# Performance work log

Hardware: AMD Instinct MI355X
Metric: run time of the kernel (lower is better)

## Reference

```python
import jax, jax.numpy as jnp
import numpy as np

# --- model dims (match init_kwargs) ---
B, N = 2, 4096          # batch, seq_len
D = 1024                # model dim
H, DH = 16, 64          # heads, dim_head (inner = H*DH = D)
R = 64                  # num_random_features
L = 6                   # depth
FF = 4 * D              # ff_dim
V = 32000               # vocab_size
MAXN = 4096             # max_seq_len
EPS = 1e-5              # torch LayerNorm default eps
STAB = 1e-6             # numerical_stabilizer
INNER = H * DH


def _ln(x, g, b):
    m = jnp.mean(x, axis=-1, keepdims=True)
    v = jnp.mean(jnp.square(x - m), axis=-1, keepdims=True)
    return (x - m) * jax.lax.rsqrt(v + EPS) * g + b


def setup_inputs() -> dict:
    key = jax.random.key(0)
    ks = jax.random.split(key, 16)
    s = 0.02
    return {
        "tokens": jax.random.randint(ks[0], (B, N), 0, V),
        "tok_emb": jax.random.normal(ks[1], (V, D), jnp.float32) * s,
        "pos_emb": jax.random.normal(ks[2], (MAXN, D), jnp.float32) * s,
        "Wqkv": jax.random.normal(ks[3], (L, 3 * INNER, D), jnp.float32) * s,
        "Wout": jax.random.normal(ks[4], (L, D, INNER), jnp.float32) * s,
        "bout": jnp.zeros((L, D), jnp.float32),
        "ln1_g": jnp.ones((L, D), jnp.float32),
        "ln1_b": jnp.zeros((L, D), jnp.float32),
        "ln2_g": jnp.ones((L, D), jnp.float32),
        "ln2_b": jnp.zeros((L, D), jnp.float32),
        "W1": jax.random.normal(ks[5], (L, FF, D), jnp.float32) * s,
        "b1": jnp.zeros((L, FF), jnp.float32),
        "W2": jax.random.normal(ks[6], (L, D, FF), jnp.float32) * s,
        "b2": jnp.zeros((L, D), jnp.float32),
        # random_features buffer: randn / sqrt(R)
        "rf": jax.random.normal(ks[7], (L, H, DH, R), jnp.float32) / np.sqrt(R),
    }


def reference(tokens, tok_emb, pos_emb, Wqkv, Wout, bout,
              ln1_g, ln1_b, ln2_g, ln2_b, W1, b1, W2, b2, rf):
    b, n = tokens.shape
    x = tok_emb[tokens] + pos_emb[jnp.arange(n)][None]  # [b,n,D]
    for l in range(L):
        # --- Performer attention (FAVOR+ linear path, ReLU kernel) ---
        h = _ln(x, ln1_g[l], ln1_b[l])
        qkv = h @ Wqkv[l].T                                  # [b,n,3*INNER]
        q, k, v = jnp.split(qkv, 3, axis=-1)
        resh = lambda t: t.reshape(b, n, H, DH).transpose(0, 2, 1, 3)  # [b,h,n,d]
        q, k, v = resh(q), resh(k), resh(v)
        phi_q = jax.nn.relu(jnp.einsum('bhnd,hdr->bhnr', q, rf[l]))
        phi_k = jax.nn.relu(jnp.einsum('bhnd,hdr->bhnr', k, rf[l]))
        kv = jnp.einsum('bhnr,bhnd->bhrd', phi_k, v)          # [b,h,r,d]
        out = jnp.einsum('bhnr,bhrd->bhnd', phi_q, kv)        # [b,h,n,d]
        # normalizer = phi_q . (sum_m phi_k)
        normz = jnp.einsum('bhnr,bhr->bhn', phi_q, phi_k.sum(axis=2))[..., None] + STAB
        out = out / normz
        out = out.transpose(0, 2, 1, 3).reshape(b, n, INNER)
        x = x + (out @ Wout[l].T + bout[l])
        # --- FFN (GELU exact, matching torch nn.GELU) ---
        h2 = _ln(x, ln2_g[l], ln2_b[l])
        ff = jax.nn.gelu(h2 @ W1[l].T + b1[l], approximate=False) @ W2[l].T + b2[l]
        x = x + ff
    return x
```

## Files before the change

kernel.cpp:

```cpp
#include <hip/hip_runtime.h>
#include <hip/hip_bf16.h>
#include <math.h>

#define NL 6
#define DMODEL 1024
#define NHEAD 16
#define MTOT 8192
#define NSEQ 4096
#define FFDIM 4096

typedef __attribute__((ext_vector_type(8))) short bf16x8;
typedef __attribute__((ext_vector_type(4))) short s16x4;
typedef __attribute__((ext_vector_type(4))) float f32x4;

__device__ __forceinline__ float b2f(short s) {
    unsigned int u = ((unsigned int)(unsigned short)s) << 16;
    return __uint_as_float(u);
}
__device__ __forceinline__ short f2b(float f) {
    __hip_bfloat16 h = __float2bfloat16(f);
    return *reinterpret_cast<short*>(&h);
}
__device__ __forceinline__ f32x4 mfma16(bf16x8 a, bf16x8 b, f32x4 c) {
    return __builtin_amdgcn_mfma_f32_16x16x32_bf16(a, b, c, 0, 0, 0);
}
__device__ __forceinline__ void gload16(const void* g, void* lds) {
    __builtin_amdgcn_global_load_lds((__attribute__((address_space(1))) void*)(g),
                                     (__attribute__((address_space(3))) void*)(lds), 16, 0, 0);
}

__global__ __launch_bounds__(256) void cvt_f2b_kernel(const float* __restrict__ in,
        short* __restrict__ out, int n4) {
    int i = blockIdx.x * 256 + threadIdx.x;
    if (i >= n4) return;
    float4 v = ((const float4*)in)[i];
    s16x4 o;
    o[0] = f2b(v.x); o[1] = f2b(v.y); o[2] = f2b(v.z); o[3] = f2b(v.w);
    ((s16x4*)out)[i] = o;
}

__global__ __launch_bounds__(256) void embed_kernel(const int* __restrict__ tok,
        const float* __restrict__ te, const float* __restrict__ pe, float* __restrict__ x) {
    int row = blockIdx.x, tid = threadIdx.x;
    int t = tok[row], n = row & (NSEQ - 1);
    float4 a = ((const float4*)(te + (size_t)t * DMODEL))[tid];
    float4 p = ((const float4*)(pe + (size_t)n * DMODEL))[tid];
    float4 o;
    o.x = a.x + p.x; o.y = a.y + p.y; o.z = a.z + p.z; o.w = a.w + p.w;
    ((float4*)(x + (size_t)row * DMODEL))[tid] = o;
}

__global__ __launch_bounds__(256) void prep_phi(const float* __restrict__ Wqkv,
        const float* __restrict__ rf, short* __restrict__ Wcomb) {
    int b = blockIdx.x;
    int kc = b & 3, qk = (b >> 2) & 1, h = (b >> 3) & 15, l = b >> 7;
    int tid = threadIdx.x;
    __shared__ float rfl[64 * 64];
    const float* rfg = rf + ((size_t)(l * NHEAD + h)) * 4096;
    #pragma unroll
    for (int u = 0; u < 4; u++) {
        int i4 = u * 256 + tid;
        ((float4*)rfl)[i4] = ((const float4*)rfg)[i4];
    }
    __syncthreads();
    int k = kc * 256 + tid;
    const float* wq = Wqkv + ((size_t)(l * 3072 + qk * 1024 + h * 64)) * DMODEL + k;
    float acc[64];
    #pragma unroll
    for (int r = 0; r < 64; r++) acc[r] = 0.f;
    #pragma unroll 4
    for (int d = 0; d < 64; d++) {
        float wd = wq[(size_t)d * DMODEL];
        const float4* rrow = (const float4*)&rfl[d * 64];
        #pragma unroll
        for (int r4 = 0; r4 < 16; r4++) {
            float4 f = rrow[r4];
            acc[r4 * 4 + 0] += f.x * wd;
            acc[r4 * 4 + 1] += f.y * wd;
            acc[r4 * 4 + 2] += f.z * wd;
            acc[r4 * 4 + 3] += f.w * wd;
        }
    }
    size_t outbase = ((size_t)(l * 3072 + qk * 1024 + h * 64)) * DMODEL + k;
    #pragma unroll
    for (int r = 0; r < 64; r++)
        Wcomb[outbase + (size_t)r * DMODEL] = f2b(acc[r]);
}

__global__ __launch_bounds__(256) void prep_v(const float* __restrict__ Wqkv,
        short* __restrict__ Wcomb) {
    int b = blockIdx.x;
    int l = b >> 10, row = b & 1023;
    int tid = threadIdx.x;
    size_t base = ((size_t)(l * 3072 + 2048 + row)) * DMODEL;
    float4 v = ((const float4*)(Wqkv + base))[tid];
    s16x4 o;
    o[0] = f2b(v.x); o[1] = f2b(v.y); o[2] = f2b(v.z); o[3] = f2b(v.w);
    ((s16x4*)(Wcomb + base))[tid] = o;
}

__global__ __launch_bounds__(256) void ln_kernel(const float* __restrict__ x,
        const float* __restrict__ g, const float* __restrict__ bta, short* __restrict__ h) {
    int row = blockIdx.x, tid = threadIdx.x, lane = tid & 63, w = tid >> 6;
    float4 v = ((const float4*)(x + (size_t)row * DMODEL))[tid];
    float s = v.x + v.y + v.z + v.w;
    float sq = v.x * v.x + v.y * v.y + v.z * v.z + v.w * v.w;
    #pragma unroll
    for (int off = 32; off > 0; off >>= 1) { s += __shfl_down(s, off); sq += __shfl_down(sq, off); }
    __shared__ float ss[4], sqq[4];
    if (lane == 0) { ss[w] = s; sqq[w] = sq; }
    __syncthreads();
    float st = ss[0] + ss[1] + ss[2] + ss[3];
    float sqt = sqq[0] + sqq[1] + sqq[2] + sqq[3];
    float mean = st * (1.f / 1024.f);
    float var = sqt * (1.f / 1024.f) - mean * mean;
    float rstd = rsqrtf(var + 1e-5f);
    int col = tid * 4;
    float4 gg = ((const float4*)g)[tid];
    float4 bb = ((const float4*)bta)[tid];
    s16x4 o;
    o[0] = f2b((v.x - mean) * rstd * gg.x + bb.x);
    o[1] = f2b((v.y - mean) * rstd * gg.y + bb.y);
    o[2] = f2b((v.z - mean) * rstd * gg.z + bb.z);
    o[3] = f2b((v.w - mean) * rstd * gg.w + bb.w);
    *(s16x4*)&h[(size_t)row * DMODEL + col] = o;
}

#define EPI_QKV 0
#define EPI_BIASRES 1
#define EPI_GELU 2

template <int EPI>
__global__ __launch_bounds__(256, 3) void gemm_bt(const short* __restrict__ A,
        const short* __restrict__ B, int K, int N,
        const float* __restrict__ bias, float* __restrict__ resx,
        short* __restrict__ out0, short* __restrict__ out1, short* __restrict__ out2) {
    __shared__ short As[128 * 64];
    __shared__ short Bs[128 * 64];
    const int tid = threadIdx.x;
    const int lane = tid & 63;
    const int w = tid >> 6;
    const int bn = blockIdx.x, bm = blockIdx.y;
    const int warow = (w >> 1) * 64;
    const int wacol = (w & 1) * 64;
    const int q = lane >> 4;

    f32x4 acc[4][4];
    #pragma unroll
    for (int i = 0; i < 4; i++)
        #pragma unroll
        for (int j = 0; j < 4; j++)
            #pragma unroll
            for (int c = 0; c < 4; c++) acc[i][j][c] = 0.f;

    unsigned aOff[4], bOff[4];
    short* ldsA[4];
    short* ldsB[4];
    #pragma unroll
    for (int i = 0; i < 4; i++) {
        int s = i * 256 + tid;
        int row = s >> 3, cp = s & 7;
        int j = cp ^ ((row >> 1) & 7);
        aOff[i] = (unsigned)((bm * 128 + row) * K + j * 8);
        bOff[i] = (unsigned)((bn * 128 + row) * K + j * 8);
        ldsA[i] = &As[s * 8];
        ldsB[i] = &Bs[s * 8];
    }

    for (int k0 = 0; k0 < K; k0 += 64) {
        #pragma unroll
        for (int i = 0; i < 4; i++) gload16(A + aOff[i] + k0, ldsA[i]);
        #pragma unroll
        for (int i = 0; i < 4; i++) gload16(B + bOff[i] + k0, ldsB[i]);
        __syncthreads();
        #pragma unroll
        for (int ksub = 0; ksub < 2; ksub++) {
            bf16x8 af[4], bfr[4];
            #pragma unroll
            for (int mt = 0; mt < 4; mt++) {
                int m = warow + mt * 16 + (lane & 15);
                int c = (ksub * 4 + q) ^ ((m >> 1) & 7);
                af[mt] = *(const bf16x8*)&As[m * 64 + c * 8];
            }
            #pragma unroll
            for (int nt = 0; nt < 4; nt++) {
                int n = wacol + nt * 16 + (lane & 15);
                int c = (ksub * 4 + q) ^ ((n >> 1) & 7);
                bfr[nt] = *(const bf16x8*)&Bs[n * 64 + c * 8];
            }
            #pragma unroll
            for (int mt = 0; mt < 4; mt++)
                #pragma unroll
                for (int nt = 0; nt < 4; nt++)
                    acc[mt][nt] = mfma16(af[mt], bfr[nt], acc[mt][nt]);
        }
        __syncthreads();
    }

    #pragma unroll
    for (int mt = 0; mt < 4; mt++) {
        int row0 = bm * 128 + warow + mt * 16 + (q << 2);
        #pragma unroll
        for (int nt = 0; nt < 4; nt++) {
            int col = bn * 128 + wacol + nt * 16 + (lane & 15);
            f32x4 v = acc[mt][nt];
            if (EPI == EPI_QKV) {
                if (col < 1024) {
                    #pragma unroll
                    for (int i = 0; i < 4; i++)
                        out0[(size_t)(row0 + i) * DMODEL + col] = f2b(fmaxf(v[i], 0.f));
                } else if (col < 2048) {
                    int c = col - 1024, hh = c >> 6, r = c & 63;
                    int b = row0 >> 12, n0 = row0 & (NSEQ - 1);
                    s16x4 pk;
                    #pragma unroll
                    for (int i = 0; i < 4; i++) pk[i] = f2b(fmaxf(v[i], 0.f));
                    *(s16x4*)&out1[((size_t)((b * NHEAD + hh) * 64 + r)) * NSEQ + n0] = pk;
                } else {
                    int c = col - 2048, hh = c >> 6, dd = c & 63;
                    int b = row0 >> 12, n0 = row0 & (NSEQ - 1);
                    s16x4 pk;
                    #pragma unroll
                    for (int i = 0; i < 4; i++) pk[i] = f2b(v[i]);
                    *(s16x4*)&out2[((size_t)((b * NHEAD + hh) * 64 + dd)) * NSEQ + n0] = pk;
                }
            } else if (EPI == EPI_BIASRES) {
                float bb = bias[col];
                #pragma unroll
                for (int i = 0; i < 4; i++) {
                    size_t idx = (size_t)(row0 + i) * N + col;
                    resx[idx] += v[i] + bb;
                }
            } else {
                float bb = bias[col];
                #pragma unroll
                for (int i = 0; i < 4; i++) {
                    float t = v[i] + bb;
                    float gg = 0.5f * t * (1.f + erff(t * 0.70710678118654752f));
                    out0[(size_t)(row0 + i) * N + col] = f2b(gg);
                }
            }
        }
    }
}

__global__ __launch_bounds__(256) void zero_kvs(float* kvs) {
    int i = blockIdx.x * 256 + threadIdx.x;
    if (i < 32 * 65 * 64) kvs[i] = 0.f;
}

__global__ __launch_bounds__(256) void kv_kernel(const short* __restrict__ phiKT,
        const short* __restrict__ vT, float* __restrict__ kvs) {
    int bh = blockIdx.x;
    int kc = blockIdx.y;
    int tid = threadIdx.x, lane = tid & 63, w = tid >> 6, q = lane >> 4;
    f32x4 acc[4];
    #pragma unroll
    for (int nt = 0; nt < 4; nt++)
        #pragma unroll
        for (int c = 0; c < 4; c++) acc[nt][c] = 0.f;
    const short* Abase = vT + ((size_t)(bh * 64 + w * 16 + (lane & 15))) * NSEQ;
    for (int ks = 0; ks < 16; ks++) {
        int k0 = kc * 512 + ks * 32 + q * 8;
        bf16x8 a = *(const bf16x8*)&Abase[k0];
        #pragma unroll
        for (int nt = 0; nt < 4; nt++) {
            bf16x8 b = *(const bf16x8*)&phiKT[((size_t)(bh * 64 + nt * 16 + (lane & 15))) * NSEQ + k0];
            acc[nt] = mfma16(a, b, acc[nt]);
        }
    }
    #pragma unroll
    for (int nt = 0; nt < 4; nt++)
        #pragma unroll
        for (int i = 0; i < 4; i++)
            atomicAdd(&kvs[((size_t)bh * 65 + (w * 16 + q * 4 + i)) * 64 + nt * 16 + (lane & 15)],
                      acc[nt][i]);
    int r = tid & 63, qq = tid >> 6;
    const short* p = phiKT + ((size_t)(bh * 64 + r)) * NSEQ + kc * 512 + qq * 128;
    float s = 0.f;
    #pragma unroll 8
    for (int u = 0; u < 128; u++) s += b2f(p[u]);
    __shared__ float red[256];
    red[tid] = s;
    __syncthreads();
    if (tid < 64) {
        float t = red[tid] + red[tid + 64] + red[tid + 128] + red[tid + 192];
        atomicAdd(&kvs[((size_t)bh * 65 + 64) * 64 + tid], t);
    }
}

__global__ __launch_bounds__(256) void cvt_kvs(const float* __restrict__ kvs,
        short* __restrict__ kvsb) {
    int bh = blockIdx.x, tid = threadIdx.x;
    for (int idx = tid; idx < 80 * 64; idx += 256) {
        int row = idx >> 6, col = idx & 63;
        float v = (row < 65) ? kvs[((size_t)bh * 65 + row) * 64 + col] : 0.f;
        kvsb[((size_t)bh * 80 + row) * 64 + col] = f2b(v);
    }
}

__global__ __launch_bounds__(256) void attn_kernel(const short* __restrict__ phiQ,
        const short* __restrict__ kvsb, short* __restrict__ attnO) {
    int mt = blockIdx.x;
    int bh = blockIdx.y;
    int b = bh >> 4, h = bh & 15;
    int tid = threadIdx.x, lane = tid & 63, w = tid >> 6, q = lane >> 4;
    int mrow = mt * 64 + w * 16 + (lane & 15);
    const short* Abase = phiQ + ((size_t)(b * NSEQ + mrow)) * DMODEL + h * 64;
    f32x4 acc[5];
    #pragma unroll
    for (int nt = 0; nt < 5; nt++)
        #pragma unroll
        for (int c = 0; c < 4; c++) acc[nt][c] = 0.f;
    #pragma unroll
    for (int k0 = 0; k0 < 64; k0 += 32) {
        bf16x8 a = *(const bf16x8*)&Abase[k0 + q * 8];
        #pragma unroll
        for (int nt = 0; nt < 5; nt++) {
            bf16x8 bb = *(const bf16x8*)&kvsb[((size_t)bh * 80 + nt * 16 + (lane & 15)) * 64 + k0 + q * 8];
            acc[nt] = mfma16(a, bb, acc[nt]);
        }
    }
    int n0 = mt * 64 + w * 16 + q * 4;
    #pragma unroll
    for (int i = 0; i < 4; i++) {
        float nz = __shfl(acc[4][i], (lane & 48)) + 1e-6f;
        #pragma unroll
        for (int nt = 0; nt < 4; nt++) {
            float val = acc[nt][i] / nz;
            attnO[((size_t)(b * NSEQ + n0 + i)) * DMODEL + h * 64 + nt * 16 + (lane & 15)] = f2b(val);
        }
    }
}

__global__ __launch_bounds__(256) void cvt_out(const float* __restrict__ x,
        float* __restrict__ out) {
    size_t i = (size_t)blockIdx.x * 256 + threadIdx.x;
    ((float4*)out)[i] = ((const float4*)x)[i];
}

extern "C" void kernel_launch(void* const* d_in, const int* in_sizes, int n_in,
                              void* d_out, int out_size, void* d_ws, size_t ws_size,
                              hipStream_t stream) {
    const int* tokens = (const int*)d_in[0];
    const float* tok_emb = (const float*)d_in[1];
    const float* pos_emb = (const float*)d_in[2];
    const float* Wqkv = (const float*)d_in[3];
    const float* Wout = (const float*)d_in[4];
    const float* bout = (const float*)d_in[5];
    const float* ln1g = (const float*)d_in[6];
    const float* ln1b = (const float*)d_in[7];
    const float* ln2g = (const float*)d_in[8];
    const float* ln2b = (const float*)d_in[9];
    const float* W1 = (const float*)d_in[10];
    const float* b1 = (const float*)d_in[11];
    const float* W2 = (const float*)d_in[12];
    const float* b2 = (const float*)d_in[13];
    const float* rf = (const float*)d_in[14];

    char* ws = (char*)d_ws;
    float* x      = (float*)ws;
    short* Wcomb  = (short*)(ws + 33554432);
    short* WoutB  = (short*)(ws + 71303168);
    short* W1B    = (short*)(ws + 83886080);
    short* W2B    = (short*)(ws + 134217728);
    short* h      = (short*)(ws + 184549376);
    short* phiQ   = (short*)(ws + 201326592);
    short* phiKT  = (short*)(ws + 218103808);
    short* vT     = (short*)(ws + 234881024);
    short* attnO  = (short*)(ws + 251658240);
    short* ff     = phiQ;
    float* kvs    = (float*)(ws + 268435456);
    short* kvsb   = (short*)(ws + 268967936);

    embed_kernel<<<MTOT, 256, 0, stream>>>(tokens, tok_emb, pos_emb, x);
    prep_phi<<<768, 256, 0, stream>>>(Wqkv, rf, Wcomb);
    prep_v<<<NL * 1024, 256, 0, stream>>>(Wqkv, Wcomb);
    cvt_f2b_kernel<<<(NL * 1024 * 1024 / 4 + 255) / 256, 256, 0, stream>>>(Wout, WoutB, NL * 1024 * 1024 / 4);
    cvt_f2b_kernel<<<(NL * 4096 * 1024 / 4 + 255) / 256, 256, 0, stream>>>(W1, W1B, NL * 4096 * 1024 / 4);
    cvt_f2b_kernel<<<(NL * 1024 * 4096 / 4 + 255) / 256, 256, 0, stream>>>(W2, W2B, NL * 1024 * 4096 / 4);

    for (int l = 0; l < NL; l++) {
        ln_kernel<<<MTOT, 256, 0, stream>>>(x, ln1g + l * 1024, ln1b + l * 1024, h);
        gemm_bt<EPI_QKV><<<dim3(24, 64), 256, 0, stream>>>(
            h, Wcomb + (size_t)l * 3072 * 1024, 1024, 3072,
            nullptr, nullptr, phiQ, phiKT, vT);
        zero_kvs<<<520, 256, 0, stream>>>(kvs);
        kv_kernel<<<dim3(32, 8), 256, 0, stream>>>(phiKT, vT, kvs);
        cvt_kvs<<<32, 256, 0, stream>>>(kvs, kvsb);
        attn_kernel<<<dim3(64, 32), 256, 0, stream>>>(phiQ, kvsb, attnO);
        gemm_bt<EPI_BIASRES><<<dim3(8, 64), 256, 0, stream>>>(
            attnO, WoutB + (size_t)l * 1024 * 1024, 1024, 1024,
            bout + l * 1024, x, nullptr, nullptr, nullptr);
        ln_kernel<<<MTOT, 256, 0, stream>>>(x, ln2g + l * 1024, ln2b + l * 1024, h);
        gemm_bt<EPI_GELU><<<dim3(32, 64), 256, 0, stream>>>(
            h, W1B + (size_t)l * 4096 * 1024, 1024, 4096,
            b1 + l * 4096, nullptr, ff, nullptr, nullptr);
        gemm_bt<EPI_BIASRES><<<dim3(8, 64), 256, 0, stream>>>(
            ff, W2B + (size_t)l * 1024 * 4096, 4096, 1024,
            b2 + l * 1024, x, nullptr, nullptr, nullptr);
    }
    cvt_out<<<MTOT * DMODEL / 1024, 256, 0, stream>>>(x, (float*)d_out);
}
```

Before: 2.613 ms.

## Double-buffer GEMM LDS tiles with BK=32 to overlap loads and MFMA

The bf16 GEMM kernel moves from a single 128x64 LDS tile per operand with two barriers per step to two 128x32 buffers. The next tile's global-to-LDS copy is issued before computing on the current one, with one barrier per iteration. The aim is to hide global load latency behind the MFMA work. The trade-off is a halved K step, which means more loop iterations and barriers and fewer MFMAs per synchronisation, with the same total LDS footprint.

```diff
diff --git a/kernel.cpp b/kernel.cpp
--- a/kernel.cpp
+++ b/kernel.cpp
@@ -135,8 +135,8 @@
         const short* __restrict__ B, int K, int N,
         const float* __restrict__ bias, float* __restrict__ resx,
         short* __restrict__ out0, short* __restrict__ out1, short* __restrict__ out2) {
-    __shared__ short As[128 * 64];
-    __shared__ short Bs[128 * 64];
+    __shared__ short As[2][128 * 32];
+    __shared__ short Bs[2][128 * 32];
     const int tid = threadIdx.x;
     const int lane = tid & 63;
     const int w = tid >> 6;
@@ -153,53 +153,55 @@
             #pragma unroll
             for (int c = 0; c < 4; c++) acc[i][j][c] = 0.f;
 
-    unsigned aOff[4], bOff[4];
-    short* ldsA[4];
-    short* ldsB[4];
-    #pragma unroll
-    for (int i = 0; i < 4; i++) {
-        int s = i * 256 + tid;
-        int row = s >> 3, cp = s & 7;
-        int j = cp ^ ((row >> 1) & 7);
-        aOff[i] = (unsigned)((bm * 128 + row) * K + j * 8);
-        bOff[i] = (unsigned)((bn * 128 + row) * K + j * 8);
-        ldsA[i] = &As[s * 8];
-        ldsB[i] = &Bs[s * 8];
-    }
-
-    for (int k0 = 0; k0 < K; k0 += 64) {
-        #pragma unroll
-        for (int i = 0; i < 4; i++) gload16(A + aOff[i] + k0, ldsA[i]);
-        #pragma unroll
-        for (int i = 0; i < 4; i++) gload16(B + bOff[i] + k0, ldsB[i]);
+    const int s0 = tid, s1 = 256 + tid;
+    const int row0 = s0 >> 2, row1 = s1 >> 2;
+    const int j0 = (s0 & 3) ^ ((row0 >> 1) & 3);
+    const int j1 = (s1 & 3) ^ ((row1 >> 1) & 3);
+    const size_t aOff0 = (size_t)(bm * 128 + row0) * K + j0 * 8;
+    const size_t aOff1 = (size_t)(bm * 128 + row1) * K + j1 * 8;
+    const size_t bOff0 = (size_t)(bn * 128 + row0) * K + j0 * 8;
+    const size_t bOff1 = (size_t)(bn * 128 + row1) * K + j1 * 8;
+
+    gload16(A + aOff0, &As[0][s0 * 8]);
+    gload16(A + aOff1, &As[0][s1 * 8]);
+    gload16(B + bOff0, &Bs[0][s0 * 8]);
+    gload16(B + bOff1, &Bs[0][s1 * 8]);
+
+    const int nk = K >> 5;
+    #pragma unroll 2
+    for (int kt = 0; kt < nk; kt++) {
+        const int cur = kt & 1, nxt = cur ^ 1;
         __syncthreads();
-        #pragma unroll
-        for (int ksub = 0; ksub < 2; ksub++) {
-            bf16x8 af[4], bfr[4];
+        if (kt + 1 < nk) {
+            const int k0 = (kt + 1) * 32;
+            gload16(A + aOff0 + k0, &As[nxt][s0 * 8]);
+            gload16(A + aOff1 + k0, &As[nxt][s1 * 8]);
+            gload16(B + bOff0 + k0, &Bs[nxt][s0 * 8]);
+            gload16(B + bOff1 + k0, &Bs[nxt][s1 * 8]);
+        }
+        bf16x8 af[4], bfr[4];
+        #pragma unroll
+        for (int mt = 0; mt < 4; mt++) {
+            int m = warow + mt * 16 + (lane & 15);
+            int c = q ^ ((m >> 1) & 3);
+            af[mt] = *(const bf16x8*)&As[cur][m * 32 + c * 8];
+        }
+        #pragma unroll
+        for (int nt = 0; nt < 4; nt++) {
+            int n = wacol + nt * 16 + (lane & 15);
+            int c = q ^ ((n >> 1) & 3);
+            bfr[nt] = *(const bf16x8*)&Bs[cur][n * 32 + c * 8];
+        }
+        #pragma unroll
+        for (int mt = 0; mt < 4; mt++)
             #pragma unroll
-            for (int mt = 0; mt < 4; mt++) {
-                int m = warow + mt * 16 + (lane & 15);
-                int c = (ksub * 4 + q) ^ ((m >> 1) & 7);
-                af[mt] = *(const bf16x8*)&As[m * 64 + c * 8];
-            }
-            #pragma unroll
-            for (int nt = 0; nt < 4; nt++) {
-                int n = wacol + nt * 16 + (lane & 15);
-                int c = (ksub * 4 + q) ^ ((n >> 1) & 7);
-                bfr[nt] = *(const bf16x8*)&Bs[n * 64 + c * 8];
-            }
-            #pragma unroll
-            for (int mt = 0; mt < 4; mt++)
-                #pragma unroll
-                for (int nt = 0; nt < 4; nt++)
-                    acc[mt][nt] = mfma16(af[mt], bfr[nt], acc[mt][nt]);
-        }
-        __syncthreads();
+            for (int nt = 0; nt < 4; nt++)
+                acc[mt][nt] = mfma16(af[mt], bfr[nt], acc[mt][nt]);
     }
 
     #pragma unroll
     for (int mt = 0; mt < 4; mt++) {
-        int row0 = bm * 128 + warow + mt * 16 + (q << 2);
+        int row0e = bm * 128 + warow + mt * 16 + (q << 2);
         #pragma unroll
         for (int nt = 0; nt < 4; nt++) {
             int col = bn * 128 + wacol + nt * 16 + (lane & 15);
@@ -208,17 +210,17 @@
                 if (col < 1024) {
                     #pragma unroll
                     for (int i = 0; i < 4; i++)
-                        out0[(size_t)(row0 + i) * DMODEL + col] = f2b(fmaxf(v[i], 0.f));
+                        out0[(size_t)(row0e + i) * DMODEL + col] = f2b(fmaxf(v[i], 0.f));
                 } else if (col < 2048) {
                     int c = col - 1024, hh = c >> 6, r = c & 63;
-                    int b = row0 >> 12, n0 = row0 & (NSEQ - 1);
+                    int b = row0e >> 12, n0 = row0e & (NSEQ - 1);
                     s16x4 pk;
                     #pragma unroll
                     for (int i = 0; i < 4; i++) pk[i] = f2b(fmaxf(v[i], 0.f));
                     *(s16x4*)&out1[((size_t)((b * NHEAD + hh) * 64 + r)) * NSEQ + n0] = pk;
                 } else {
                     int c = col - 2048, hh = c >> 6, dd = c & 63;
-                    int b = row0 >> 12, n0 = row0 & (NSEQ - 1);
+                    int b = row0e >> 12, n0 = row0e & (NSEQ - 1);
                     s16x4 pk;
                     #pragma unroll
                     for (int i = 0; i < 4; i++) pk[i] = f2b(v[i]);
@@ -228,7 +230,7 @@
                 float bb = bias[col];
                 #pragma unroll
                 for (int i = 0; i < 4; i++) {
-                    size_t idx = (size_t)(row0 + i) * N + col;
+                    size_t idx = (size_t)(row0e + i) * N + col;
                     resx[idx] += v[i] + bb;
                 }
             } else {
@@ -237,7 +239,7 @@
                 for (int i = 0; i < 4; i++) {
                     float t = v[i] + bb;
                     float gg = 0.5f * t * (1.f + erff(t * 0.70710678118654752f));
-                    out0[(size_t)(row0 + i) * N + col] = f2b(gg);
+                    out0[(size_t)(row0e + i) * N + col] = f2b(gg);
                 }
             }
         }
```

After: 2.792 ms. +6.8%, slower.
